# Kernel tuning notes

Hardware: AMD Instinct MI355X
Metric: run time of the kernel (lower is better)

## Reference

```python
import jax, jax.numpy as jnp
import numpy as np

B, F, V = 64, 256, 128   # groups, frames/group, vecs/group (uniform ragged groups)
CF = 512                 # cross_feature


def setup_inputs() -> dict:
    key = jax.random.key(0)
    ks = jax.random.split(key, 18)
    p = lambda k, s: jax.random.normal(k, s, jnp.float32) * 0.02
    return {
        "metas": jax.random.uniform(ks[0], (B, 5), jnp.float32),
        "meta_indexs": jnp.arange(B),
        "frames": jax.random.normal(ks[1], (B * F, 600), jnp.float32),
        "frame_indexs": jnp.repeat(jnp.arange(B), F),
        "vecs": jax.random.normal(ks[2], (B * V, 768), jnp.float32),
        "vec_indexs": jnp.repeat(jnp.arange(B), V),
        "audios": jax.random.normal(ks[3], (B, 128), jnp.float32),
        "audio_indexs": jnp.arange(B),
        "Wfk": p(ks[4], (CF, 600)), "Wfv": p(ks[5], (CF, 600)),
        "Wvk": p(ks[6], (CF, 768)), "Wvv": p(ks[7], (CF, 768)),
        "Wav": p(ks[8], (CF, 128)),
        "Wff_f": p(ks[9], (2, CF, CF)),
        "Wff_v": p(ks[10], (2, CF, CF)),
        "Wff_a": p(ks[11], (2, CF, CF)),
        "Wout1": p(ks[12], (768, 3 * CF + 3)),
        "Wout2": p(ks[13], (512, 768)),
        "Wout3": p(ks[14], (64, 512)),
        "Wout4": p(ks[15], (1, 64)),
    }


def reference(metas, meta_indexs, frames, frame_indexs, vecs, vec_indexs,
              audios, audio_indexs, Wfk, Wfv, Wvk, Wvv, Wav,
              Wff_f, Wff_v, Wff_a, Wout1, Wout2, Wout3, Wout4):
    # groups are uniform: reshape ragged rows into [B, n, d] (indexes are
    # contiguous repeats per setup_inputs, so the mask-gathers become reshapes)
    b = audios.shape[0]
    fb = frames.reshape(b, -1, frames.shape[-1])   # [B,F,600]
    vb = vecs.reshape(b, -1, vecs.shape[-1])       # [B,V,768]
    relu = jax.nn.relu

    f_k = relu(jnp.einsum('bfd,cd->bfc', fb, Wfk))     # [B,F,CF]
    f_v = relu(jnp.einsum('bfd,cd->bfc', fb, Wfv))
    v_k = relu(jnp.einsum('bvd,cd->bvc', vb, Wvk))     # [B,V,CF]
    v_v = relu(jnp.einsum('bvd,cd->bvc', vb, Wvv))
    a_v = relu(audios @ Wav.T)                         # [B,CF]

    # torch: softmax(mm(k, q)) with no dim on an (N,1) tensor -> dim=1 -> ones,
    # so the initial "attended" queries are plain sums of the value projections.
    f_q_p = f_v.sum(axis=1)                            # [B,CF]
    v_q_p = v_v.sum(axis=1)
    a_q_p = a_v                                        # single audio row

    for i in range(2):
        attn_f = jax.nn.softmax(jnp.einsum('bfc,bc->bf', f_k, v_q_p) / CF, axis=1)
        f_c = jnp.einsum('bf,bfc->bc', attn_f, f_v)
        f_q_n = f_c @ Wff_f[i].T + f_q_p
        attn_v = jax.nn.softmax(jnp.einsum('bvc,bc->bv', v_k, v_q_p) / CF, axis=1)
        v_c = jnp.einsum('bv,bvc->bc', attn_v, v_v)
        v_q_n = v_c @ Wff_v[i].T + v_q_p
        # audio attention is softmax over a single element -> weight 1
        a_q_n = a_v @ Wff_a[i].T + a_q_p
        f_q_p, v_q_p, a_q_p = f_q_n, v_q_n, a_q_n      # dropout is dead code

    mean = a_q_p.mean(axis=1, keepdims=True)
    std = a_q_p.std(axis=1, keepdims=True, ddof=1)     # torch.std is unbiased
    na = (a_q_p - mean) / std

    goal = metas[:, 1:2] / 1500.0
    dura = metas[:, 3:4] - metas[:, 2:3]
    dura = jnp.where(dura > 8000.0, 100.0, dura) / 100.0
    create = metas[:, 4:5] / 5.0

    feats = jnp.concatenate([f_q_p, v_q_p, na, goal, create, dura], axis=1)  # [B,1539]
    h = relu(feats @ Wout1.T)
    h = relu(h @ Wout2.T)
    h = relu(h @ Wout3.T)
    out = jax.nn.sigmoid(h @ Wout4.T)                  # [B,1]
    return out[:, 0]
```

## Files before the change

kernel.cpp:

```cpp
#include <hip/hip_runtime.h>
#include <hip/hip_bf16.h>

typedef __attribute__((ext_vector_type(4))) float f32x4;
typedef __attribute__((ext_vector_type(8))) __bf16 bf16x8;
typedef __attribute__((ext_vector_type(4))) unsigned short us4;
typedef __attribute__((ext_vector_type(8))) unsigned short us8;
typedef __attribute__((ext_vector_type(4))) unsigned int u32x4;

#define LDS_AS __attribute__((address_space(3)))
#define GLB_AS __attribute__((address_space(1)))

__device__ __forceinline__ unsigned short f2bf(float f) {
    unsigned u = __builtin_bit_cast(unsigned, f);
    return (unsigned short)((u + 0x7FFFu + ((u >> 16) & 1u)) >> 16);
}
__device__ __forceinline__ float bf2f(unsigned short h) {
    return __builtin_bit_cast(float, (unsigned)h << 16);
}
__device__ __forceinline__ void cp16(const void* g, void* l) {
    __builtin_amdgcn_global_load_lds((const GLB_AS unsigned int*)g,
                                     (LDS_AS unsigned int*)l, 16, 0, 0);
}

#define NPREP 10112
__global__ __launch_bounds__(256) void prep_kernel(
    const float* __restrict__ frames, const float* __restrict__ Wfk, const float* __restrict__ Wfv,
    const float* __restrict__ vecs, const float* __restrict__ Wvk, const float* __restrict__ Wvv,
    const float* __restrict__ Wout1, const float* __restrict__ audios, const float* __restrict__ Wav,
    unsigned short* __restrict__ fbf, unsigned short* __restrict__ wf,
    unsigned short* __restrict__ vbf, unsigned short* __restrict__ wv,
    float* __restrict__ W1p, float* __restrict__ hacc, float* __restrict__ qz,
    float* __restrict__ a_v, float* __restrict__ a_q_p)
{
    __shared__ float aud[128];
    const int t = threadIdx.x;
    if (blockIdx.x >= NPREP) {
        const int b = blockIdx.x - NPREP;
        if (t < 128) aud[t] = audios[b * 128 + t];
        __syncthreads();
        #pragma unroll
        for (int cc = 0; cc < 2; ++cc) {
            int c = 2 * t + cc;
            const float* wr = Wav + (size_t)c * 128;
            float s = 0.f;
            #pragma unroll
            for (int k4 = 0; k4 < 32; ++k4) {
                f32x4 wvv = *(const f32x4*)(wr + k4 * 4);
                s += wvv[0] * aud[k4 * 4] + wvv[1] * aud[k4 * 4 + 1]
                   + wvv[2] * aud[k4 * 4 + 2] + wvv[3] * aud[k4 * 4 + 3];
            }
            s = s > 0.f ? s : 0.f;
            a_v[b * 512 + c] = s;
            a_q_p[b * 512 + c] = s;
        }
        return;
    }
    int i = blockIdx.x * 256 + t;
    if (i < 1245184) {
        int row = i / 76, k = (i - row * 76) * 8;
        us8 o = {0, 0, 0, 0, 0, 0, 0, 0};
        if (k < 600) {
            const float* s = frames + (size_t)row * 600 + k;
            f32x4 v0 = *(const f32x4*)s;
            f32x4 v1 = *(const f32x4*)(s + 4);
            o[0] = f2bf(v0[0]); o[1] = f2bf(v0[1]); o[2] = f2bf(v0[2]); o[3] = f2bf(v0[3]);
            o[4] = f2bf(v1[0]); o[5] = f2bf(v1[1]); o[6] = f2bf(v1[2]); o[7] = f2bf(v1[3]);
        }
        *(us8*)(fbf + (size_t)row * 608 + k) = o;
        return;
    }
    i -= 1245184;
    if (i < 77824) {
        int row = i / 76, k = (i - row * 76) * 8;
        const float* src = row < 512 ? Wfk + (size_t)row * 600 : Wfv + (size_t)(row - 512) * 600;
        us8 o = {0, 0, 0, 0, 0, 0, 0, 0};
        if (k < 600) {
            f32x4 v0 = *(const f32x4*)(src + k);
            f32x4 v1 = *(const f32x4*)(src + k + 4);
            o[0] = f2bf(v0[0]); o[1] = f2bf(v0[1]); o[2] = f2bf(v0[2]); o[3] = f2bf(v0[3]);
            o[4] = f2bf(v1[0]); o[5] = f2bf(v1[1]); o[6] = f2bf(v1[2]); o[7] = f2bf(v1[3]);
        }
        *(us8*)(wf + (size_t)row * 608 + k) = o;
        return;
    }
    i -= 77824;
    if (i < 786432) {
        int row = i / 96, k = (i - row * 96) * 8;
        const float* s = vecs + (size_t)row * 768 + k;
        f32x4 v0 = *(const f32x4*)s;
        f32x4 v1 = *(const f32x4*)(s + 4);
        us8 o = {f2bf(v0[0]), f2bf(v0[1]), f2bf(v0[2]), f2bf(v0[3]),
                 f2bf(v1[0]), f2bf(v1[1]), f2bf(v1[2]), f2bf(v1[3])};
        *(us8*)(vbf + (size_t)row * 768 + k) = o;
        return;
    }
    i -= 786432;
    if (i < 98304) {
        int row = i / 96, k = (i - row * 96) * 8;
        const float* src = (row < 512 ? Wvk + (size_t)row * 768
                                      : Wvv + (size_t)(row - 512) * 768) + k;
        f32x4 v0 = *(const f32x4*)src;
        f32x4 v1 = *(const f32x4*)(src + 4);
        us8 o = {f2bf(v0[0]), f2bf(v0[1]), f2bf(v0[2]), f2bf(v0[3]),
                 f2bf(v1[0]), f2bf(v1[1]), f2bf(v1[2]), f2bf(v1[3])};
        *(us8*)(wv + (size_t)row * 768 + k) = o;
        return;
    }
    i -= 98304;
    if (i < 344064) {
        int r = i / 448, k = (i - r * 448) * 4;
        f32x4 o;
        #pragma unroll
        for (int j = 0; j < 4; ++j) {
            int kk = k + j;
            o[j] = kk < 1539 ? Wout1[(size_t)r * 1539 + kk] : 0.f;
        }
        *(f32x4*)(W1p + (size_t)r * 1792 + k) = o;
        return;
    }
    i -= 344064;
    if (i < 20480) {
        f32x4 z = {0, 0, 0, 0};
        *(f32x4*)(hacc + (size_t)i * 4) = z;
        return;
    }
    i -= 20480;
    if (i < 16384) {
        f32x4 z = {0, 0, 0, 0};
        *(f32x4*)(qz + (size_t)i * 4) = z;
    }
}

__global__ __launch_bounds__(256) void gemm_bt_relu(
    const unsigned short* __restrict__ A, const unsigned short* __restrict__ B,
    unsigned short* __restrict__ C, int Kp, float* __restrict__ qout, int gshift)
{
    __shared__ alignas(16) unsigned short sA[128 * 32];
    __shared__ alignas(16) unsigned short sB[128 * 32];
    const int t = threadIdx.x;
    const int w = t >> 6, l = t & 63;
    const int nwg = gridDim.x;
    const int swz = (blockIdx.x & 7) * (nwg >> 3) + (blockIdx.x >> 3);
    const int bm = swz >> 3, bn = swz & 7;
    const int m0 = bm << 7, n0 = bn << 7;

    const int srow = t >> 2, sk0 = (t & 3) << 3;
    const unsigned short* gA = A + (size_t)(m0 + srow) * Kp + sk0;
    const unsigned short* gB = B + (size_t)(n0 + srow) * Kp + sk0;
    char* lA = (char*)sA + w * 1024;
    char* lB = (char*)sB + w * 1024;

    const int wr = w >> 1, wc = w & 1;
    const unsigned short* pA = sA + (size_t)((wr * 64 + (l & 15)) * 32 + ((l >> 4) << 3));
    const unsigned short* pB = sB + (size_t)((wc * 64 + (l & 15)) * 32 + ((l >> 4) << 3));

    f32x4 acc[4][4] = {};
    const int ksteps = Kp >> 5;
    for (int kt = 0; kt < ksteps; ++kt) {
        const unsigned short* ga = gA + kt * 32;
        const unsigned short* gb = gB + kt * 32;
        cp16(ga, lA);
        cp16(ga + (size_t)64 * Kp, lA + 4096);
        cp16(gb, lB);
        cp16(gb + (size_t)64 * Kp, lB + 4096);
        __syncthreads();
        bf16x8 af[4], bfr[4];
        #pragma unroll
        for (int i = 0; i < 4; ++i) {
            af[i]  = *(const bf16x8*)(pA + i * 512);
            bfr[i] = *(const bf16x8*)(pB + i * 512);
        }
        #pragma unroll
        for (int mi = 0; mi < 4; ++mi)
            #pragma unroll
            for (int ni = 0; ni < 4; ++ni)
                acc[mi][ni] = __builtin_amdgcn_mfma_f32_16x16x32_bf16(af[mi], bfr[ni], acc[mi][ni], 0, 0, 0);
        __syncthreads();
    }
    const int crow0 = m0 + wr * 64 + ((l >> 4) << 2);
    const int ccol0 = n0 + wc * 64 + (l & 15);
    #pragma unroll
    for (int mi = 0; mi < 4; ++mi)
        #pragma unroll
        for (int ni = 0; ni < 4; ++ni)
            #pragma unroll
            for (int j = 0; j < 4; ++j) {
                float v = acc[mi][ni][j];
                v = v > 0.f ? v : 0.f;
                C[(size_t)(crow0 + mi * 16 + j) * 1024 + (ccol0 + ni * 16)] = f2bf(v);
            }
    if (n0 >= 512) {
        const int g = m0 >> gshift;
        float csum[4];
        #pragma unroll
        for (int ni = 0; ni < 4; ++ni) {
            float s = 0.f;
            #pragma unroll
            for (int mi = 0; mi < 4; ++mi)
                #pragma unroll
                for (int j = 0; j < 4; ++j)
                    s += fmaxf(acc[mi][ni][j], 0.f);
            s += __shfl_xor(s, 16, 64);
            s += __shfl_xor(s, 32, 64);
            csum[ni] = s;
        }
        if (l < 16) {
            #pragma unroll
            for (int ni = 0; ni < 4; ++ni)
                atomicAdd(&qout[g * 512 + (ccol0 - 512) + ni * 16], csum[ni]);
        }
    }
}

__global__ __launch_bounds__(256) void scores_kernel(
    const unsigned short* __restrict__ Cf, const unsigned short* __restrict__ Cv,
    const float* __restrict__ v_q_p, float* __restrict__ sbuf, float* __restrict__ fvz)
{
    const int t = threadIdx.x, bid = blockIdx.x;
    if (bid < 64) {
        f32x4 z = {0, 0, 0, 0};
        ((f32x4*)fvz)[bid * 256 + t] = z;
    }
    const int w = t >> 6, l = t & 63;
    int frame, g, soff;
    const unsigned short* X;
    if (bid < 4096) { frame = bid * 4 + w; g = frame >> 8; X = Cf; soff = 0; }
    else            { frame = (bid - 4096) * 4 + w; g = frame >> 7; X = Cv; soff = 16384; }
    const float* vq = v_q_p + g * 512 + l * 8;
    f32x4 q0 = *(const f32x4*)vq;
    f32x4 q1 = *(const f32x4*)(vq + 4);
    u32x4 u = *(const u32x4*)(X + (size_t)frame * 1024 + l * 8);
    float acc = q0[0] * bf2f((unsigned short)(u[0] & 0xffff)) + q0[1] * bf2f((unsigned short)(u[0] >> 16))
              + q0[2] * bf2f((unsigned short)(u[1] & 0xffff)) + q0[3] * bf2f((unsigned short)(u[1] >> 16))
              + q1[0] * bf2f((unsigned short)(u[2] & 0xffff)) + q1[1] * bf2f((unsigned short)(u[2] >> 16))
              + q1[2] * bf2f((unsigned short)(u[3] & 0xffff)) + q1[3] * bf2f((unsigned short)(u[3] >> 16));
    #pragma unroll
    for (int m = 1; m < 64; m <<= 1) acc += __shfl_xor(acc, m, 64);
    if (l == 0) sbuf[soff + frame] = acc * (1.f / 512.f);
}

__global__ __launch_bounds__(256) void pv_kernel(
    const unsigned short* __restrict__ Cf, const unsigned short* __restrict__ Cv,
    const float* __restrict__ sbuf, float* __restrict__ fc, float* __restrict__ vc)
{
    __shared__ float ws[256];
    __shared__ float red[256];
    const int t = threadIdx.x, bid = blockIdx.x;
    int g, chunk, NF, soff;
    const unsigned short* X;
    float* outp;
    if (bid < 512) { g = bid >> 3; chunk = bid & 7; NF = 256; X = Cf; soff = g * 256; outp = fc; }
    else { int b2 = bid - 512; g = b2 >> 2; chunk = b2 & 3; NF = 128; X = Cv; soff = 16384 + g * 128; outp = vc; }
    float s = (t < NF) ? sbuf[soff + t] : -1e30f;
    red[t] = s;
    __syncthreads();
    for (int st = 128; st > 0; st >>= 1) { if (t < st) red[t] = fmaxf(red[t], red[t + st]); __syncthreads(); }
    float m = red[0];
    __syncthreads();
    float e = (t < NF) ? __expf(s - m) : 0.f;
    ws[t] = e;
    red[t] = e;
    __syncthreads();
    for (int st = 128; st > 0; st >>= 1) { if (t < st) red[t] += red[t + st]; __syncthreads(); }
    float inv = 1.f / red[0];
    const int f0 = g * NF + chunk * 32;
    const unsigned int* q = (const unsigned int*)X + (size_t)f0 * 512 + 256 + t;
    float s0 = 0.f, s1 = 0.f;
    #pragma unroll 4
    for (int f = 0; f < 32; ++f) {
        float a = ws[chunk * 32 + f];
        unsigned u = q[(size_t)f * 512];
        s0 += a * bf2f((unsigned short)(u & 0xffff));
        s1 += a * bf2f((unsigned short)(u >> 16));
    }
    atomicAdd(&outp[g * 512 + 2 * t],     s0 * inv);
    atomicAdd(&outp[g * 512 + 2 * t + 1], s1 * inv);
}

__device__ __forceinline__ void gemv_body(
    const float* __restrict__ X, int ldx, int dorelu,
    const float* __restrict__ W, int ldw, float* __restrict__ Y, int ldy,
    int nc, int kc, int bc)
{
    __shared__ float xs[4096];
    const int t = threadIdx.x;
    #pragma unroll
    for (int j = 0; j < 16; ++j) {
        int idx = t + j * 256;
        float v = X[(size_t)(bc * 32 + (idx >> 7)) * ldx + kc * 128 + (idx & 127)];
        xs[idx] = dorelu ? (v > 0.f ? v : 0.f) : v;
    }
    __syncthreads();
    const int r = t & 63, bg = t >> 6;
    const int row = nc * 64 + r;
    const float* wrow = W + (size_t)row * ldw + kc * 128;
    float acc[8] = {};
    #pragma unroll 8
    for (int k4 = 0; k4 < 32; ++k4) {
        f32x4 wvv = *(const f32x4*)(wrow + k4 * 4);
        #pragma unroll
        for (int bb = 0; bb < 8; ++bb) {
            f32x4 xv = *(const f32x4*)(xs + (bg * 8 + bb) * 128 + k4 * 4);
            acc[bb] += wvv[0] * xv[0] + wvv[1] * xv[1] + wvv[2] * xv[2] + wvv[3] * xv[3];
        }
    }
    #pragma unroll
    for (int bb = 0; bb < 8; ++bb)
        atomicAdd(&Y[(size_t)(bc * 32 + bg * 8 + bb) * ldy + row], acc[bb]);
}

__global__ __launch_bounds__(256) void update_kernel(
    const float* __restrict__ Wff_f, const float* __restrict__ Wff_v, const float* __restrict__ Wff_a,
    int iter, const float* __restrict__ fc, const float* __restrict__ vc, const float* __restrict__ a_v,
    float* __restrict__ f_q_p, float* __restrict__ v_q_p, float* __restrict__ a_q_p)
{
    int id = blockIdx.x;
    const int op = id >> 6; id &= 63;
    const int nc = id & 7, kc = (id >> 3) & 3, bc = id >> 5;
    const float* W = (op == 0 ? Wff_f : op == 1 ? Wff_v : Wff_a) + (size_t)iter * 262144;
    const float* X = op == 0 ? fc : op == 1 ? vc : a_v;
    float* Y = op == 0 ? f_q_p : op == 1 ? v_q_p : a_q_p;
    gemv_body(X, 512, 0, W, 512, Y, 512, nc, kc, bc);
}

__global__ __launch_bounds__(256) void gemvb_kernel(
    const float* __restrict__ X, int ldx, int dorelu,
    const float* __restrict__ W, int ldw, float* __restrict__ Y, int ldy,
    int NC, int KC)
{
    int bid = blockIdx.x;
    const int nc = bid % NC; bid /= NC;
    const int kc = bid % KC;
    const int bc = bid / KC;
    gemv_body(X, ldx, dorelu, W, ldw, Y, ldy, nc, kc, bc);
}

__global__ __launch_bounds__(512) void normfeats_kernel(
    const float* __restrict__ a_q_p, const float* __restrict__ f_q_p, const float* __restrict__ v_q_p,
    const float* __restrict__ metas, float* __restrict__ feats)
{
    __shared__ float red[512];
    const int t = threadIdx.x, b = blockIdx.x;
    float a = a_q_p[b * 512 + t];
    red[t] = a;
    __syncthreads();
    for (int s = 256; s > 0; s >>= 1) { if (t < s) red[t] += red[t + s]; __syncthreads(); }
    float mean = red[0] * (1.f / 512.f);
    __syncthreads();
    float d = a - mean;
    red[t] = d * d;
    __syncthreads();
    for (int s = 256; s > 0; s >>= 1) { if (t < s) red[t] += red[t + s]; __syncthreads(); }
    float sd = sqrtf(red[0] * (1.f / 511.f));
    float* fr = feats + (size_t)b * 1792;
    fr[t]        = f_q_p[b * 512 + t];
    fr[512 + t]  = v_q_p[b * 512 + t];
    fr[1024 + t] = d / sd;
    if (t < 256) {
        float v = 0.f;
        if (t == 0) v = metas[b * 5 + 1] * (1.f / 1500.f);
        else if (t == 1) v = metas[b * 5 + 4] * 0.2f;
        else if (t == 2) {
            float du = metas[b * 5 + 3] - metas[b * 5 + 2];
            v = (du > 8000.f ? 100.f : du) * 0.01f;
        }
        fr[1536 + t] = v;
    }
}

__global__ __launch_bounds__(256) void mlp34_kernel(
    const float* __restrict__ h2acc, const float* __restrict__ W3, const float* __restrict__ W4,
    float* __restrict__ out)
{
    __shared__ float xs[512];
    __shared__ float part[256];
    __shared__ float h3[64];
    const int t = threadIdx.x, b = blockIdx.x;
    {
        float v0 = h2acc[(size_t)b * 512 + t];
        float v1 = h2acc[(size_t)b * 512 + 256 + t];
        xs[t] = v0 > 0.f ? v0 : 0.f;
        xs[256 + t] = v1 > 0.f ? v1 : 0.f;
    }
    __syncthreads();
    const int r = t & 63, q = t >> 6;
    const float* wrow = W3 + (size_t)r * 512 + q * 128;
    float acc = 0.f;
    #pragma unroll 8
    for (int k4 = 0; k4 < 32; ++k4) {
        f32x4 wvv = *(const f32x4*)(wrow + k4 * 4);
        f32x4 xv  = *(const f32x4*)(xs + q * 128 + k4 * 4);
        acc += wvv[0] * xv[0] + wvv[1] * xv[1] + wvv[2] * xv[2] + wvv[3] * xv[3];
    }
    part[t] = acc;
    __syncthreads();
    if (t < 64) {
        float h = part[t] + part[t + 64] + part[t + 128] + part[t + 192];
        h3[t] = h > 0.f ? h : 0.f;
    }
    __syncthreads();
    if (t < 64) {
        float v = h3[t] * W4[t];
        #pragma unroll
        for (int m = 1; m < 64; m <<= 1) v += __shfl_xor(v, m, 64);
        if (t == 0) out[b] = 1.f / (1.f + __expf(-v));
    }
}

extern "C" void kernel_launch(void* const* d_in, const int* in_sizes, int n_in,
                              void* d_out, int out_size, void* d_ws, size_t ws_size,
                              hipStream_t stream)
{
    const float* metas  = (const float*)d_in[0];
    const float* frames = (const float*)d_in[2];
    const float* vecs   = (const float*)d_in[4];
    const float* audios = (const float*)d_in[6];
    const float* Wfk   = (const float*)d_in[8];
    const float* Wfv   = (const float*)d_in[9];
    const float* Wvk   = (const float*)d_in[10];
    const float* Wvv   = (const float*)d_in[11];
    const float* Wav   = (const float*)d_in[12];
    const float* Wff_f = (const float*)d_in[13];
    const float* Wff_v = (const float*)d_in[14];
    const float* Wff_a = (const float*)d_in[15];
    const float* Wout1 = (const float*)d_in[16];
    const float* Wout2 = (const float*)d_in[17];
    const float* Wout3 = (const float*)d_in[18];
    const float* Wout4 = (const float*)d_in[19];
    float* out = (float*)d_out;

    char* p = (char*)d_ws;
    auto alloc = [&](size_t n) { char* r = p; p += (n + 255) & ~(size_t)255; return r; };
    unsigned short* fbf = (unsigned short*)alloc(16384ull * 608 * 2);
    unsigned short* wf  = (unsigned short*)alloc(1024ull * 608 * 2);
    unsigned short* vbf = (unsigned short*)alloc(8192ull * 768 * 2);
    unsigned short* wv  = (unsigned short*)alloc(1024ull * 768 * 2);
    unsigned short* Cf  = (unsigned short*)alloc(16384ull * 1024 * 2);
    unsigned short* Cv  = (unsigned short*)alloc(8192ull * 1024 * 2);
    float* W1p   = (float*)alloc(768ull * 1792 * 4);
    float* feats = (float*)alloc(64ull * 1792 * 4);
    float* qbuf  = (float*)alloc(2ull * 64 * 512 * 4);
    float* f_q_p = qbuf;
    float* v_q_p = qbuf + 64 * 512;
    float* a_q_p = (float*)alloc(64ull * 512 * 4);
    float* a_v   = (float*)alloc(64ull * 512 * 4);
    float* fvc   = (float*)alloc(2ull * 64 * 512 * 4);
    float* fcb   = fvc;
    float* vcb   = fvc + 64 * 512;
    float* hacc  = (float*)alloc(81920ull * 4);
    float* h1acc = hacc;
    float* h2acc = hacc + 64 * 768;
    float* sbuf  = (float*)alloc(24576ull * 4);

    prep_kernel<<<NPREP + 64, 256, 0, stream>>>(frames, Wfk, Wfv, vecs, Wvk, Wvv, Wout1,
                                                audios, Wav, fbf, wf, vbf, wv, W1p, hacc,
                                                qbuf, a_v, a_q_p);
    gemm_bt_relu<<<1024, 256, 0, stream>>>(fbf, wf, Cf, 608, f_q_p, 8);
    gemm_bt_relu<<<512, 256, 0, stream>>>(vbf, wv, Cv, 768, v_q_p, 7);
    for (int i = 0; i < 2; ++i) {
        scores_kernel<<<6144, 256, 0, stream>>>(Cf, Cv, v_q_p, sbuf, fvc);
        pv_kernel<<<768, 256, 0, stream>>>(Cf, Cv, sbuf, fcb, vcb);
        update_kernel<<<192, 256, 0, stream>>>(Wff_f, Wff_v, Wff_a, i, fcb, vcb, a_v,
                                               f_q_p, v_q_p, a_q_p);
    }
    normfeats_kernel<<<64, 512, 0, stream>>>(a_q_p, f_q_p, v_q_p, metas, feats);
    gemvb_kernel<<<336, 256, 0, stream>>>(feats, 1792, 0, W1p, 1792, h1acc, 768, 12, 14);
    gemvb_kernel<<<96, 256, 0, stream>>>(h1acc, 768, 1, Wout2, 768, h2acc, 512, 8, 6);
    mlp34_kernel<<<64, 256, 0, stream>>>(h2acc, Wout3, Wout4, out);
}
```

Baseline: 189.8 us.

## Fuse fp32-to-bf16 activation conversion into projection GEMM with double-buffered LDS

Removes the separate bf16 copies of frames and vecs produced in the prep kernel. The projection GEMM now reads fp32 activations directly, converts them to bf16 in registers and stores them to LDS, so the intermediate bf16 buffers are no longer written and read back through HBM. It also double-buffers the A and B tiles so the loads for the next k-step overlap the MFMA work of the current one. In exchange the GEMM loads twice the A bytes as fp32 and does the conversion inside the main loop, and LDS use per block doubles.

```diff
diff --git a/kernel.cpp b/kernel.cpp
--- a/kernel.cpp
+++ b/kernel.cpp
@@ -3,7 +3,6 @@
 
 typedef __attribute__((ext_vector_type(4))) float f32x4;
 typedef __attribute__((ext_vector_type(8))) __bf16 bf16x8;
-typedef __attribute__((ext_vector_type(4))) unsigned short us4;
 typedef __attribute__((ext_vector_type(8))) unsigned short us8;
 typedef __attribute__((ext_vector_type(4))) unsigned int u32x4;
 
@@ -22,20 +21,20 @@
                                      (LDS_AS unsigned int*)l, 16, 0, 0);
 }
 
-#define NPREP 10112
+#define NPREPB 544
+#define NTOT 557056
 __global__ __launch_bounds__(256) void prep_kernel(
-    const float* __restrict__ frames, const float* __restrict__ Wfk, const float* __restrict__ Wfv,
-    const float* __restrict__ vecs, const float* __restrict__ Wvk, const float* __restrict__ Wvv,
+    const float* __restrict__ Wfk, const float* __restrict__ Wfv,
+    const float* __restrict__ Wvk, const float* __restrict__ Wvv,
     const float* __restrict__ Wout1, const float* __restrict__ audios, const float* __restrict__ Wav,
-    unsigned short* __restrict__ fbf, unsigned short* __restrict__ wf,
-    unsigned short* __restrict__ vbf, unsigned short* __restrict__ wv,
+    unsigned short* __restrict__ wf, unsigned short* __restrict__ wv,
     float* __restrict__ W1p, float* __restrict__ hacc, float* __restrict__ qz,
     float* __restrict__ a_v, float* __restrict__ a_q_p)
 {
     __shared__ float aud[128];
     const int t = threadIdx.x;
-    if (blockIdx.x >= NPREP) {
-        const int b = blockIdx.x - NPREP;
+    if (blockIdx.x >= NPREPB) {
+        const int b = blockIdx.x - NPREPB;
         if (t < 128) aud[t] = audios[b * 128 + t];
         __syncthreads();
         #pragma unroll
@@ -55,88 +54,66 @@
         }
         return;
     }
-    int i = blockIdx.x * 256 + t;
-    if (i < 1245184) {
-        int row = i / 76, k = (i - row * 76) * 8;
-        us8 o = {0, 0, 0, 0, 0, 0, 0, 0};
-        if (k < 600) {
-            const float* s = frames + (size_t)row * 600 + k;
-            f32x4 v0 = *(const f32x4*)s;
-            f32x4 v1 = *(const f32x4*)(s + 4);
-            o[0] = f2bf(v0[0]); o[1] = f2bf(v0[1]); o[2] = f2bf(v0[2]); o[3] = f2bf(v0[3]);
-            o[4] = f2bf(v1[0]); o[5] = f2bf(v1[1]); o[6] = f2bf(v1[2]); o[7] = f2bf(v1[3]);
-        }
-        *(us8*)(fbf + (size_t)row * 608 + k) = o;
-        return;
-    }
-    i -= 1245184;
-    if (i < 77824) {
-        int row = i / 76, k = (i - row * 76) * 8;
-        const float* src = row < 512 ? Wfk + (size_t)row * 600 : Wfv + (size_t)(row - 512) * 600;
-        us8 o = {0, 0, 0, 0, 0, 0, 0, 0};
-        if (k < 600) {
-            f32x4 v0 = *(const f32x4*)(src + k);
-            f32x4 v1 = *(const f32x4*)(src + k + 4);
-            o[0] = f2bf(v0[0]); o[1] = f2bf(v0[1]); o[2] = f2bf(v0[2]); o[3] = f2bf(v0[3]);
-            o[4] = f2bf(v1[0]); o[5] = f2bf(v1[1]); o[6] = f2bf(v1[2]); o[7] = f2bf(v1[3]);
-        }
-        *(us8*)(wf + (size_t)row * 608 + k) = o;
-        return;
-    }
-    i -= 77824;
-    if (i < 786432) {
-        int row = i / 96, k = (i - row * 96) * 8;
-        const float* s = vecs + (size_t)row * 768 + k;
-        f32x4 v0 = *(const f32x4*)s;
-        f32x4 v1 = *(const f32x4*)(s + 4);
-        us8 o = {f2bf(v0[0]), f2bf(v0[1]), f2bf(v0[2]), f2bf(v0[3]),
-                 f2bf(v1[0]), f2bf(v1[1]), f2bf(v1[2]), f2bf(v1[3])};
-        *(us8*)(vbf + (size_t)row * 768 + k) = o;
-        return;
-    }
-    i -= 786432;
-    if (i < 98304) {
-        int row = i / 96, k = (i - row * 96) * 8;
-        const float* src = (row < 512 ? Wvk + (size_t)row * 768
-                                      : Wvv + (size_t)(row - 512) * 768) + k;
-        f32x4 v0 = *(const f32x4*)src;
-        f32x4 v1 = *(const f32x4*)(src + 4);
-        us8 o = {f2bf(v0[0]), f2bf(v0[1]), f2bf(v0[2]), f2bf(v0[3]),
-                 f2bf(v1[0]), f2bf(v1[1]), f2bf(v1[2]), f2bf(v1[3])};
-        *(us8*)(wv + (size_t)row * 768 + k) = o;
-        return;
-    }
-    i -= 98304;
-    if (i < 344064) {
-        int r = i / 448, k = (i - r * 448) * 4;
-        f32x4 o;
-        #pragma unroll
-        for (int j = 0; j < 4; ++j) {
-            int kk = k + j;
-            o[j] = kk < 1539 ? Wout1[(size_t)r * 1539 + kk] : 0.f;
-        }
-        *(f32x4*)(W1p + (size_t)r * 1792 + k) = o;
-        return;
-    }
-    i -= 344064;
-    if (i < 20480) {
-        f32x4 z = {0, 0, 0, 0};
-        *(f32x4*)(hacc + (size_t)i * 4) = z;
-        return;
-    }
-    i -= 20480;
-    if (i < 16384) {
-        f32x4 z = {0, 0, 0, 0};
-        *(f32x4*)(qz + (size_t)i * 4) = z;
-    }
-}
-
-__global__ __launch_bounds__(256) void gemm_bt_relu(
-    const unsigned short* __restrict__ A, const unsigned short* __restrict__ B,
+    for (int i = blockIdx.x * 256 + t; i < NTOT; i += NPREPB * 256) {
+        int idx = i;
+        if (idx < 77824) {
+            int row = idx / 76, k = (idx - row * 76) * 8;
+            const float* src = row < 512 ? Wfk + (size_t)row * 600 : Wfv + (size_t)(row - 512) * 600;
+            us8 o = {0, 0, 0, 0, 0, 0, 0, 0};
+            if (k < 600) {
+                f32x4 v0 = *(const f32x4*)(src + k);
+                f32x4 v1 = *(const f32x4*)(src + k + 4);
+                o[0] = f2bf(v0[0]); o[1] = f2bf(v0[1]); o[2] = f2bf(v0[2]); o[3] = f2bf(v0[3]);
+                o[4] = f2bf(v1[0]); o[5] = f2bf(v1[1]); o[6] = f2bf(v1[2]); o[7] = f2bf(v1[3]);
+            }
+            *(us8*)(wf + (size_t)row * 608 + k) = o;
+            continue;
+        }
+        idx -= 77824;
+        if (idx < 98304) {
+            int row = idx / 96, k = (idx - row * 96) * 8;
+            const float* src = (row < 512 ? Wvk + (size_t)row * 768
+                                          : Wvv + (size_t)(row - 512) * 768) + k;
+            f32x4 v0 = *(const f32x4*)src;
+            f32x4 v1 = *(const f32x4*)(src + 4);
+            us8 o = {f2bf(v0[0]), f2bf(v0[1]), f2bf(v0[2]), f2bf(v0[3]),
+                     f2bf(v1[0]), f2bf(v1[1]), f2bf(v1[2]), f2bf(v1[3])};
+            *(us8*)(wv + (size_t)row * 768 + k) = o;
+            continue;
+        }
+        idx -= 98304;
+        if (idx < 344064) {
+            int r = idx / 448, k = (idx - r * 448) * 4;
+            f32x4 o;
+            #pragma unroll
+            for (int j = 0; j < 4; ++j) {
+                int kk = k + j;
+                o[j] = kk < 1539 ? Wout1[(size_t)r * 1539 + kk] : 0.f;
+            }
+            *(f32x4*)(W1p + (size_t)r * 1792 + k) = o;
+            continue;
+        }
+        idx -= 344064;
+        if (idx < 20480) {
+            f32x4 z = {0, 0, 0, 0};
+            *(f32x4*)(hacc + (size_t)idx * 4) = z;
+            continue;
+        }
+        idx -= 20480;
+        {
+            f32x4 z = {0, 0, 0, 0};
+            *(f32x4*)(qz + (size_t)idx * 4) = z;
+        }
+    }
+}
+
+__global__ __launch_bounds__(256) void gemm_fused(
+    const float* __restrict__ Afp, int Kreal,
+    const unsigned short* __restrict__ B,
     unsigned short* __restrict__ C, int Kp, float* __restrict__ qout, int gshift)
 {
-    __shared__ alignas(16) unsigned short sA[128 * 32];
-    __shared__ alignas(16) unsigned short sB[128 * 32];
+    __shared__ alignas(16) unsigned short sA[2 * 4096];
+    __shared__ alignas(16) unsigned short sB[2 * 4096];
     const int t = threadIdx.x;
     const int w = t >> 6, l = t & 63;
     const int nwg = gridDim.x;
@@ -145,25 +122,55 @@
     const int m0 = bm << 7, n0 = bn << 7;
 
     const int srow = t >> 2, sk0 = (t & 3) << 3;
-    const unsigned short* gA = A + (size_t)(m0 + srow) * Kp + sk0;
     const unsigned short* gB = B + (size_t)(n0 + srow) * Kp + sk0;
-    char* lA = (char*)sA + w * 1024;
-    char* lB = (char*)sB + w * 1024;
+    const int arow = t >> 1, ac0 = (t & 1) << 4;
+    const float* gA = Afp + (size_t)(m0 + arow) * Kreal + ac0;
 
     const int wr = w >> 1, wc = w & 1;
-    const unsigned short* pA = sA + (size_t)((wr * 64 + (l & 15)) * 32 + ((l >> 4) << 3));
-    const unsigned short* pB = sB + (size_t)((wc * 64 + (l & 15)) * 32 + ((l >> 4) << 3));
+    const int ksteps = Kp >> 5;
+
+    f32x4 av[4];
+    {
+        char* lB = (char*)sB + w * 1024;
+        cp16(gB, lB);
+        cp16(gB + (size_t)64 * Kp, lB + 4096);
+        #pragma unroll
+        for (int j = 0; j < 4; ++j) {
+            int c = ac0 + j * 4;
+            av[j] = (c < Kreal) ? *(const f32x4*)(gA + j * 4) : f32x4{0.f, 0.f, 0.f, 0.f};
+        }
+        unsigned short* dA = sA + arow * 32 + ac0;
+        #pragma unroll
+        for (int h = 0; h < 2; ++h) {
+            us8 o;
+            #pragma unroll
+            for (int e = 0; e < 8; ++e) {
+                float f = av[h * 2 + (e >> 2)][e & 3];
+                o[e] = __builtin_bit_cast(unsigned short, __float2bfloat16(f));
+            }
+            *(us8*)(dA + h * 8) = o;
+        }
+    }
+    __syncthreads();
 
     f32x4 acc[4][4] = {};
-    const int ksteps = Kp >> 5;
+    int cur = 0;
     for (int kt = 0; kt < ksteps; ++kt) {
-        const unsigned short* ga = gA + kt * 32;
-        const unsigned short* gb = gB + kt * 32;
-        cp16(ga, lA);
-        cp16(ga + (size_t)64 * Kp, lA + 4096);
-        cp16(gb, lB);
-        cp16(gb + (size_t)64 * Kp, lB + 4096);
-        __syncthreads();
+        const bool more = (kt + 1 < ksteps);
+        if (more) {
+            const unsigned short* gb = gB + (kt + 1) * 32;
+            char* lB = (char*)sB + (cur ^ 1) * 8192 + w * 1024;
+            cp16(gb, lB);
+            cp16(gb + (size_t)64 * Kp, lB + 4096);
+            #pragma unroll
+            for (int j = 0; j < 4; ++j) {
+                int c = (kt + 1) * 32 + ac0 + j * 4;
+                av[j] = (c < Kreal) ? *(const f32x4*)(gA + (kt + 1) * 32 + j * 4)
+                                    : f32x4{0.f, 0.f, 0.f, 0.f};
+            }
+        }
+        const unsigned short* pA = sA + cur * 4096 + (wr * 64 + (l & 15)) * 32 + ((l >> 4) << 3);
+        const unsigned short* pB = sB + cur * 4096 + (wc * 64 + (l & 15)) * 32 + ((l >> 4) << 3);
         bf16x8 af[4], bfr[4];
         #pragma unroll
         for (int i = 0; i < 4; ++i) {
@@ -175,8 +182,23 @@
             #pragma unroll
             for (int ni = 0; ni < 4; ++ni)
                 acc[mi][ni] = __builtin_amdgcn_mfma_f32_16x16x32_bf16(af[mi], bfr[ni], acc[mi][ni], 0, 0, 0);
+        if (more) {
+            unsigned short* dA = sA + (cur ^ 1) * 4096 + arow * 32 + ac0;
+            #pragma unroll
+            for (int h = 0; h < 2; ++h) {
+                us8 o;
+                #pragma unroll
+                for (int e = 0; e < 8; ++e) {
+                    float f = av[h * 2 + (e >> 2)][e & 3];
+                    o[e] = __builtin_bit_cast(unsigned short, __float2bfloat16(f));
+                }
+                *(us8*)(dA + h * 8) = o;
+            }
+        }
         __syncthreads();
-    }
+        cur ^= 1;
+    }
+
     const int crow0 = m0 + wr * 64 + ((l >> 4) << 2);
     const int ccol0 = n0 + wc * 64 + (l & 15);
     #pragma unroll
@@ -431,9 +453,7 @@
 
     char* p = (char*)d_ws;
     auto alloc = [&](size_t n) { char* r = p; p += (n + 255) & ~(size_t)255; return r; };
-    unsigned short* fbf = (unsigned short*)alloc(16384ull * 608 * 2);
     unsigned short* wf  = (unsigned short*)alloc(1024ull * 608 * 2);
-    unsigned short* vbf = (unsigned short*)alloc(8192ull * 768 * 2);
     unsigned short* wv  = (unsigned short*)alloc(1024ull * 768 * 2);
     unsigned short* Cf  = (unsigned short*)alloc(16384ull * 1024 * 2);
     unsigned short* Cv  = (unsigned short*)alloc(8192ull * 1024 * 2);
@@ -452,11 +472,10 @@
     float* h2acc = hacc + 64 * 768;
     float* sbuf  = (float*)alloc(24576ull * 4);
 
-    prep_kernel<<<NPREP + 64, 256, 0, stream>>>(frames, Wfk, Wfv, vecs, Wvk, Wvv, Wout1,
-                                                audios, Wav, fbf, wf, vbf, wv, W1p, hacc,
-                                                qbuf, a_v, a_q_p);
-    gemm_bt_relu<<<1024, 256, 0, stream>>>(fbf, wf, Cf, 608, f_q_p, 8);
-    gemm_bt_relu<<<512, 256, 0, stream>>>(vbf, wv, Cv, 768, v_q_p, 7);
+    prep_kernel<<<NPREPB + 64, 256, 0, stream>>>(Wfk, Wfv, Wvk, Wvv, Wout1, audios, Wav,
+                                                 wf, wv, W1p, hacc, qbuf, a_v, a_q_p);
+    gemm_fused<<<1024, 256, 0, stream>>>(frames, 600, wf, Cf, 608, f_q_p, 8);
+    gemm_fused<<<512, 256, 0, stream>>>(vecs, 768, wv, Cv, 768, v_q_p, 7);
     for (int i = 0; i < 2; ++i) {
         scores_kernel<<<6144, 256, 0, stream>>>(Cf, Cv, v_q_p, sbuf, fvc);
         pv_kernel<<<768, 256, 0, stream>>>(Cf, Cv, sbuf, fcb, vcb);
```

Result: no change. 191.7 us (+1.0%).
